# Kernel optimization log

Hardware: AMD Instinct MI355X
Metric: run time of the kernel (lower is better)

## Reference

```python
import jax, jax.numpy as jnp
import numpy as np

TEMPERATURE = 0.07
LAMBDA_CONTRASTIVE = 0.3
LAMBDA_CLASSIFICATION = 0.7
B = 8192
NUM_CLASSES = 57
EMBED_DIM = 256
NUM_TASKS = 57


def setup_inputs() -> dict:
    key = jax.random.key(0)
    k1, k2, k3, k4 = jax.random.split(key, 4)
    logits = jax.random.normal(k1, (B, NUM_CLASSES), dtype=jnp.float32)
    embeddings = jax.random.normal(k2, (B, EMBED_DIM), dtype=jnp.float32)
    labels = jax.random.randint(k3, (B,), 0, NUM_CLASSES, dtype=jnp.int64)
    task_ids = jax.random.randint(k4, (B,), 0, NUM_TASKS, dtype=jnp.int64)
    return {"logits": logits, "embeddings": embeddings, "labels": labels, "task_ids": task_ids}


def _forward(logits, embeddings, labels, task_ids):
    n, num_classes = logits.shape
    # --- classification loss (CrossEntropyLoss, mean) ---
    logp = jax.nn.log_softmax(logits, axis=-1)
    cls_loss = -jnp.take_along_axis(logp, labels[:, None], axis=1).squeeze(1).mean()
    # --- uncertainty: normalized entropy of softmax ---
    probs = jax.nn.softmax(logits, axis=-1)
    entropy = -jnp.sum(probs * jnp.log(probs + 1e-8), axis=-1)
    uncertainties = entropy / np.log(num_classes)
    # --- inter-task InfoNCE, uncertainty weighted ---
    norms = jnp.linalg.norm(embeddings, axis=-1, keepdims=True)
    e = embeddings / jnp.maximum(norms, 1e-12)  # F.normalize
    sim = jnp.matmul(e, e.T) / TEMPERATURE  # [B, B]
    eye = jnp.eye(n, dtype=bool)
    same_task = task_ids[None, :] == task_ids[:, None]
    pos_mask = same_task & ~eye          # task_mask with diagonal removed
    neg_mask = (~same_task) & ~eye       # negative_mask with diagonal removed
    exps = jnp.exp(sim)
    neg_sum = jnp.sum(jnp.where(neg_mask, exps, 0.0), axis=1)  # [B]
    valid = (pos_mask.sum(axis=1) > 0) & (neg_mask.sum(axis=1) > 0)  # [B]
    # per (anchor i, positive j): -log(exp(s_ij) / (exp(s_ij) + neg_sum_i + 1e-8)) * u_i
    pair_loss = -jnp.log(exps / (exps + neg_sum[:, None] + 1e-8)) * uncertainties[:, None]
    m = pos_mask & valid[:, None]
    count = jnp.maximum(m.sum(), 1)
    contrastive = jnp.sum(jnp.where(m, pair_loss, 0.0)) / count
    contrastive = jnp.where(m.sum() > 0, contrastive, 0.0)
    total = LAMBDA_CLASSIFICATION * cls_loss + LAMBDA_CONTRASTIVE * contrastive
    return total


def reference(logits, embeddings, labels, task_ids):
    return _forward(logits, embeddings, labels, task_ids)
```

## Files before the change

### kernel.cpp

```cpp
#include <hip/hip_runtime.h>
#include <hip/hip_fp8.h>
#include <math.h>

#define BSZ   8192
#define NCLS  57
#define DIM   256
#define NTASK 57
#define INV_T (1.0f/0.07f)
#define GBM   64
#define GBN   32
#define NTILE (GBM * GBN)
#define FINB  256

typedef float f32x4 __attribute__((ext_vector_type(4)));
typedef long  lgx2  __attribute__((ext_vector_type(2)));

__device__ __forceinline__ void gload_lds16(const void* g, void* l) {
    __builtin_amdgcn_global_load_lds(
        (const __attribute__((address_space(1))) unsigned int*)g,
        (__attribute__((address_space(3))) unsigned int*)l, 16, 0, 0);
}

__global__ __launch_bounds__(256) void k_prep(
        const float* __restrict__ logits, const float* __restrict__ emb,
        const int* __restrict__ labels, float* __restrict__ u,
        float* __restrict__ cls_part, unsigned char* __restrict__ e,
        int* __restrict__ hdr) {
    __shared__ float scls[4];
    int wave = threadIdx.x >> 6;
    int lane = threadIdx.x & 63;
    int row  = blockIdx.x * 4 + wave;

    float v = (lane < NCLS) ? logits[row * NCLS + lane] : -3.0e38f;
    float m = v;
    #pragma unroll
    for (int s = 1; s < 64; s <<= 1) m = fmaxf(m, __shfl_xor(m, s));
    float ex = (lane < NCLS) ? __expf(v - m) : 0.0f;
    float se = ex;
    #pragma unroll
    for (int s = 1; s < 64; s <<= 1) se += __shfl_xor(se, s);
    float lse = m + logf(se);
    float p = ex / se;
    float term = (lane < NCLS) ? p * logf(p + 1e-8f) : 0.0f;
    float ent = term;
    #pragma unroll
    for (int s = 1; s < 64; s <<= 1) ent += __shfl_xor(ent, s);
    ent = -ent;
    int lab = labels[row];
    float vl = __shfl(v, lab);
    float cls = lse - vl;

    const float4* src = reinterpret_cast<const float4*>(emb + (size_t)row * DIM);
    float4 x = src[lane];
    float ss = x.x*x.x + x.y*x.y + x.z*x.z + x.w*x.w;
    #pragma unroll
    for (int s = 1; s < 64; s <<= 1) ss += __shfl_xor(ss, s);
    float sc = 1.0f / fmaxf(sqrtf(ss), 1e-12f);
    __hip_fp8_e4m3 f0(x.x * sc), f1(x.y * sc), f2(x.z * sc), f3(x.w * sc);
    uchar4 o;
    o.x = *reinterpret_cast<unsigned char*>(&f0);
    o.y = *reinterpret_cast<unsigned char*>(&f1);
    o.z = *reinterpret_cast<unsigned char*>(&f2);
    o.w = *reinterpret_cast<unsigned char*>(&f3);
    int kp = (lane >> 4) * 64 + ((lane >> 1) & 3) * 16 + ((lane >> 3) & 1) * 8
           + (lane & 1) * 4;
    *reinterpret_cast<uchar4*>(e + (size_t)row * DIM + kp) = o;

    if (lane == 0) {
        u[row] = ent / 4.04305127f;
        scls[wave] = cls;
    }
    if (blockIdx.x == 0 && threadIdx.x < 64) hdr[threadIdx.x] = 0;
    __syncthreads();
    if (threadIdx.x == 0) cls_part[blockIdx.x] = scls[0] + scls[1] + scls[2] + scls[3];
}

template<bool HD>
__device__ __forceinline__ void epi_accum(
        const f32x4 (&acc)[4][4], const unsigned char* ts, const int* ctb,
        int m0, int cbase, int h, int g, int lr,
        float (&T)[4], float (&P)[4], float (&S)[4]) {
    #pragma unroll
    for (int m = 0; m < 4; ++m) {
        unsigned rt4 = *reinterpret_cast<const unsigned*>(&ts[h * 64 + m * 16 + g * 4]);
        #pragma unroll
        for (int r = 0; r < 4; ++r) {
            int rt = (rt4 >> (8 * r)) & 255;
            #pragma unroll
            for (int f = 0; f < 4; ++f) {
                float sv = acc[m][f][r] * INV_T;
                float ev = __expf(sv);
                bool keep = true;
                if (HD)
                    keep = (m0 + h * 64 + m * 16 + g * 4 + r) != (cbase + f * 16 + lr);
                bool eq = (rt == ctb[f]) && keep;
                T[f] += keep ? ev : 0.0f;
                P[f] += eq ? ev : 0.0f;
                S[f] += eq ? sv : 0.0f;
            }
        }
    }
}

__global__ __launch_bounds__(512, 2) void k_negsum(
        const unsigned char* __restrict__ E, const int* __restrict__ tasks,
        float* __restrict__ partial, int* __restrict__ task_count) {
    __shared__ unsigned char Asm[128 * 256];
    __shared__ unsigned char ts[128];
    __shared__ float scr[3][256];

    int b = (blockIdx.x & 7) * (NTILE / 8) + (blockIdx.x >> 3);
    int bm = b >> 5, bn = b & 31;
    int m0 = bm * 128, n0 = bn * 256;
    bool hasdiag = (bn == (bm >> 1));

    int tid = threadIdx.x;
    int w = tid >> 6, lane = tid & 63;
    int h = w >> 2, cg = w & 3;
    int g = lane >> 4, lr = lane & 15;
    int cbase = n0 + cg * 64;
    const unsigned char* bp = E + (size_t)(cbase + lr) * DIM + g * 16;

    lgx2 bc[4];
    #pragma unroll
    for (int f = 0; f < 4; ++f)
        bc[f] = *reinterpret_cast<const lgx2*>(bp + (size_t)f * 16 * DIM);

    #pragma unroll
    for (int it = 0; it < 4; ++it) {
        int flat = it * 512 + tid;
        int row = flat >> 4, kb = flat & 15;
        int kbs = kb ^ (row & 7);
        gload_lds16(E + (size_t)(m0 + row) * DIM + kbs * 16,
                    Asm + (size_t)(it * 512 + w * 64) * 16);
    }
    if (tid < 128) ts[tid] = (unsigned char)tasks[m0 + tid];
    __syncthreads();
    if (bn == 0 && tid < 128) atomicAdd(&task_count[ts[tid]], 1);

    f32x4 acc[4][4] = {};
    #pragma unroll 1
    for (int t = 0; t < 4; ++t) {
        lgx2 bn_[4];
        if (t < 3) {
            #pragma unroll
            for (int f = 0; f < 4; ++f)
                bn_[f] = *reinterpret_cast<const lgx2*>(
                    bp + (size_t)f * 16 * DIM + (t + 1) * 64);
        }
        lgx2 a[4];
        #pragma unroll
        for (int m = 0; m < 4; ++m)
            a[m] = *reinterpret_cast<const lgx2*>(
                Asm + (size_t)(h * 64 + m * 16 + lr) * 256
                    + (((t * 4 + g) ^ (lr & 7)) * 16));
        #pragma unroll
        for (int m = 0; m < 4; ++m)
            #pragma unroll
            for (int f = 0; f < 4; ++f) {
                acc[m][f] = __builtin_amdgcn_mfma_f32_16x16x32_fp8_fp8(
                    a[m][0], bc[f][0], acc[m][f], 0, 0, 0);
                acc[m][f] = __builtin_amdgcn_mfma_f32_16x16x32_fp8_fp8(
                    a[m][1], bc[f][1], acc[m][f], 0, 0, 0);
            }
        if (t < 3) {
            #pragma unroll
            for (int f = 0; f < 4; ++f) bc[f] = bn_[f];
        }
    }

    int ctb[4];
    #pragma unroll
    for (int f = 0; f < 4; ++f) ctb[f] = tasks[cbase + f * 16 + lr];
    float T[4] = {}, P[4] = {}, S[4] = {};
    if (hasdiag) epi_accum<true >(acc, ts, ctb, m0, cbase, h, g, lr, T, P, S);
    else         epi_accum<false>(acc, ts, ctb, m0, cbase, h, g, lr, T, P, S);

    #pragma unroll
    for (int f = 0; f < 4; ++f) {
        T[f] += __shfl_xor(T[f], 16); T[f] += __shfl_xor(T[f], 32);
        P[f] += __shfl_xor(P[f], 16); P[f] += __shfl_xor(P[f], 32);
        S[f] += __shfl_xor(S[f], 16); S[f] += __shfl_xor(S[f], 32);
    }
    if (h == 1 && g == 0) {
        #pragma unroll
        for (int f = 0; f < 4; ++f) {
            int c = cg * 64 + f * 16 + lr;
            scr[0][c] = T[f]; scr[1][c] = P[f]; scr[2][c] = S[f];
        }
    }
    __syncthreads();
    if (h == 0 && g == 0) {
        #pragma unroll
        for (int f = 0; f < 4; ++f) {
            int c = cg * 64 + f * 16 + lr;
            size_t sl = (size_t)bm * BSZ + n0 + c;
            partial[sl]                         = T[f] + scr[0][c];
            partial[(size_t)GBM * BSZ + sl]     = P[f] + scr[1][c];
            partial[(size_t)2 * GBM * BSZ + sl] = S[f] + scr[2][c];
        }
    }
}

__global__ __launch_bounds__(256) void k_finalize(
        const int* __restrict__ tasks, const int* __restrict__ task_count,
        const float* __restrict__ partial, const float* __restrict__ u,
        const float* __restrict__ cls_part, int* __restrict__ hdr,
        float* __restrict__ out) {
    __shared__ float sT[8][32], sP[8][32], sS[8][32];
    __shared__ float redf[4]; __shared__ long long redn[4];
    __shared__ int lastflag;

    int* ticket = hdr;
    float* contr_total = (float*)(hdr + 1);

    int tid = threadIdx.x;
    int c = tid & 31, q = tid >> 5;
    int j = blockIdx.x * 32 + c;

    float T = 0.0f, P = 0.0f, S = 0.0f;
    #pragma unroll
    for (int k = 0; k < 8; ++k) {
        int bm = q * 8 + k;
        size_t sl = (size_t)bm * BSZ + j;
        T += partial[sl];
        P += partial[(size_t)GBM * BSZ + sl];
        S += partial[(size_t)2 * GBM * BSZ + sl];
    }
    sT[q][c] = T; sP[q][c] = P; sS[q][c] = S;
    __syncthreads();

    if (tid < 32) {
        #pragma unroll
        for (int qq = 1; qq < 8; ++qq) {
            T = (qq == 1 ? sT[0][tid] : T) + sT[qq][tid];
            P = (qq == 1 ? sP[0][tid] : P) + sP[qq][tid];
            S = (qq == 1 ? sS[0][tid] : S) + sS[qq][tid];
        }
        int jj = blockIdx.x * 32 + tid;
        int cc = task_count[tasks[jj]];
        float v = 0.0f;
        if (cc >= 2 && cc < BSZ) {
            float C = (T - P) + 1e-8f;
            v = u[jj] * ((float)(cc - 1) * logf(C) + P / C - S);
        }
        #pragma unroll
        for (int s = 1; s < 32; s <<= 1) v += __shfl_xor(v, s);
        if (tid == 0) {
            atomicAdd(contr_total, v);
            __threadfence();
            lastflag = (__hip_atomic_fetch_add(ticket, 1, __ATOMIC_ACQ_REL,
                                               __HIP_MEMORY_SCOPE_AGENT) == FINB - 1);
        }
    }
    __syncthreads();
    if (!lastflag) return;
    __threadfence();

    float cl = 0.0f;
    for (int i = tid; i < BSZ / 4; i += 256) cl += cls_part[i];
    long long cn = 0;
    if (tid < NTASK) {
        int cc = task_count[tid];
        if (cc >= 2 && cc < BSZ) cn = (long long)cc * (cc - 1);
    }
    #pragma unroll
    for (int s = 1; s < 64; s <<= 1) { cl += __shfl_xor(cl, s); cn += __shfl_xor(cn, s); }
    int w = tid >> 6, lane = tid & 63;
    if (lane == 0) { redf[w] = cl; redn[w] = cn; }
    __syncthreads();
    if (tid == 0) {
        float ct = 0.0f; long long cnt = 0;
        #pragma unroll
        for (int qq = 0; qq < 4; ++qq) { ct += redf[qq]; cnt += redn[qq]; }
        float con = __hip_atomic_load(contr_total, __ATOMIC_ACQUIRE,
                                      __HIP_MEMORY_SCOPE_AGENT);
        out[0] = 0.7f * (ct / (float)BSZ)
               + 0.3f * (cnt > 0 ? con / (float)cnt : 0.0f);
    }
}

extern "C" void kernel_launch(void* const* d_in, const int* in_sizes, int n_in,
                              void* d_out, int out_size, void* d_ws, size_t ws_size,
                              hipStream_t stream) {
    const float* logits = (const float*)d_in[0];
    const float* emb    = (const float*)d_in[1];
    const int*   labels = (const int*)d_in[2];
    const int*   tasks  = (const int*)d_in[3];
    float* out = (float*)d_out;

    char* ws = (char*)d_ws;
    int*   hdr      = (int*)ws;
    int*   task_cnt = hdr + 2;
    float* u        = (float*)ws + 64;
    float* cls_part = u + BSZ;
    float* partial  = cls_part + 2048;
    unsigned char* e = (unsigned char*)(partial + (size_t)3 * GBM * BSZ);

    k_prep    <<<BSZ / 4, 256, 0, stream>>>(logits, emb, labels, u, cls_part, e, hdr);
    k_negsum  <<<NTILE,   512, 0, stream>>>(e, tasks, partial, task_cnt);
    k_finalize<<<FINB,    256, 0, stream>>>(tasks, task_cnt, partial, u, cls_part,
                                            hdr, out);
}
```

Baseline: 72.05 us.

## Halve row tile per block, raise occupancy, and use exp2 in epilogue

The negsum GEMM tile is cut from 128 to 64 rows per block, giving twice as many blocks. Smaller LDS and register footprints allow launch bounds of 8 blocks per SM instead of 2. The B-operand register prefetch is dropped in favour of loading directly inside the loop. The epilogue now uses exp2 with a pre-scaled constant and applies ln2 to S in finalize. In exchange, finalize reads twice as many partial rows, and more blocks reload the same B columns.

```diff
diff --git a/kernel.cpp b/kernel.cpp
--- a/kernel.cpp
+++ b/kernel.cpp
@@ -7,7 +7,9 @@
 #define DIM   256
 #define NTASK 57
 #define INV_T (1.0f/0.07f)
-#define GBM   64
+#define C2EXP (INV_T * 1.44269504f)
+#define LN2   0.69314718f
+#define GBM   128
 #define GBN   32
 #define NTILE (GBM * GBN)
 #define FINB  256
@@ -77,42 +79,42 @@
 
 template<bool HD>
 __device__ __forceinline__ void epi_accum(
-        const f32x4 (&acc)[4][4], const unsigned char* ts, const int* ctb,
+        const f32x4 (&acc)[2][4], const unsigned char* ts, const int* ctb,
         int m0, int cbase, int h, int g, int lr,
         float (&T)[4], float (&P)[4], float (&S)[4]) {
     #pragma unroll
-    for (int m = 0; m < 4; ++m) {
-        unsigned rt4 = *reinterpret_cast<const unsigned*>(&ts[h * 64 + m * 16 + g * 4]);
+    for (int m = 0; m < 2; ++m) {
+        unsigned rt4 = *reinterpret_cast<const unsigned*>(&ts[h * 32 + m * 16 + g * 4]);
         #pragma unroll
         for (int r = 0; r < 4; ++r) {
             int rt = (rt4 >> (8 * r)) & 255;
             #pragma unroll
             for (int f = 0; f < 4; ++f) {
-                float sv = acc[m][f][r] * INV_T;
-                float ev = __expf(sv);
+                float s2 = acc[m][f][r] * C2EXP;
+                float ev = exp2f(s2);
                 bool keep = true;
                 if (HD)
-                    keep = (m0 + h * 64 + m * 16 + g * 4 + r) != (cbase + f * 16 + lr);
+                    keep = (m0 + h * 32 + m * 16 + g * 4 + r) != (cbase + f * 16 + lr);
                 bool eq = (rt == ctb[f]) && keep;
                 T[f] += keep ? ev : 0.0f;
                 P[f] += eq ? ev : 0.0f;
-                S[f] += eq ? sv : 0.0f;
+                S[f] += eq ? s2 : 0.0f;
             }
         }
     }
 }
 
-__global__ __launch_bounds__(512, 2) void k_negsum(
+__global__ __launch_bounds__(512, 8) void k_negsum(
         const unsigned char* __restrict__ E, const int* __restrict__ tasks,
         float* __restrict__ partial, int* __restrict__ task_count) {
-    __shared__ unsigned char Asm[128 * 256];
-    __shared__ unsigned char ts[128];
+    __shared__ unsigned char Asm[64 * 256];
+    __shared__ unsigned char ts[64];
     __shared__ float scr[3][256];
 
     int b = (blockIdx.x & 7) * (NTILE / 8) + (blockIdx.x >> 3);
     int bm = b >> 5, bn = b & 31;
-    int m0 = bm * 128, n0 = bn * 256;
-    bool hasdiag = (bn == (bm >> 1));
+    int m0 = bm * 64, n0 = bn * 256;
+    bool hasdiag = (bn == (bm >> 2));
 
     int tid = threadIdx.x;
     int w = tid >> 6, lane = tid & 63;
@@ -121,51 +123,38 @@
     int cbase = n0 + cg * 64;
     const unsigned char* bp = E + (size_t)(cbase + lr) * DIM + g * 16;
 
-    lgx2 bc[4];
-    #pragma unroll
-    for (int f = 0; f < 4; ++f)
-        bc[f] = *reinterpret_cast<const lgx2*>(bp + (size_t)f * 16 * DIM);
-
-    #pragma unroll
-    for (int it = 0; it < 4; ++it) {
+    #pragma unroll
+    for (int it = 0; it < 2; ++it) {
         int flat = it * 512 + tid;
         int row = flat >> 4, kb = flat & 15;
         int kbs = kb ^ (row & 7);
         gload_lds16(E + (size_t)(m0 + row) * DIM + kbs * 16,
                     Asm + (size_t)(it * 512 + w * 64) * 16);
     }
-    if (tid < 128) ts[tid] = (unsigned char)tasks[m0 + tid];
-    __syncthreads();
-    if (bn == 0 && tid < 128) atomicAdd(&task_count[ts[tid]], 1);
-
-    f32x4 acc[4][4] = {};
+    if (tid < 64) ts[tid] = (unsigned char)tasks[m0 + tid];
+    __syncthreads();
+    if (bn == 0 && tid < 64) atomicAdd(&task_count[ts[tid]], 1);
+
+    f32x4 acc[2][4] = {};
     #pragma unroll 1
     for (int t = 0; t < 4; ++t) {
-        lgx2 bn_[4];
-        if (t < 3) {
+        lgx2 a[2];
+        #pragma unroll
+        for (int m = 0; m < 2; ++m)
+            a[m] = *reinterpret_cast<const lgx2*>(
+                Asm + (size_t)(h * 32 + m * 16 + lr) * 256
+                    + (((t * 4 + g) ^ (lr & 7)) * 16));
+        #pragma unroll
+        for (int f = 0; f < 4; ++f) {
+            lgx2 bc = *reinterpret_cast<const lgx2*>(
+                bp + (size_t)f * 16 * DIM + t * 64);
             #pragma unroll
-            for (int f = 0; f < 4; ++f)
-                bn_[f] = *reinterpret_cast<const lgx2*>(
-                    bp + (size_t)f * 16 * DIM + (t + 1) * 64);
-        }
-        lgx2 a[4];
-        #pragma unroll
-        for (int m = 0; m < 4; ++m)
-            a[m] = *reinterpret_cast<const lgx2*>(
-                Asm + (size_t)(h * 64 + m * 16 + lr) * 256
-                    + (((t * 4 + g) ^ (lr & 7)) * 16));
-        #pragma unroll
-        for (int m = 0; m < 4; ++m)
-            #pragma unroll
-            for (int f = 0; f < 4; ++f) {
+            for (int m = 0; m < 2; ++m) {
                 acc[m][f] = __builtin_amdgcn_mfma_f32_16x16x32_fp8_fp8(
-                    a[m][0], bc[f][0], acc[m][f], 0, 0, 0);
+                    a[m][0], bc[0], acc[m][f], 0, 0, 0);
                 acc[m][f] = __builtin_amdgcn_mfma_f32_16x16x32_fp8_fp8(
-                    a[m][1], bc[f][1], acc[m][f], 0, 0, 0);
+                    a[m][1], bc[1], acc[m][f], 0, 0, 0);
             }
-        if (t < 3) {
-            #pragma unroll
-            for (int f = 0; f < 4; ++f) bc[f] = bn_[f];
         }
     }
 
@@ -220,8 +209,8 @@
 
     float T = 0.0f, P = 0.0f, S = 0.0f;
     #pragma unroll
-    for (int k = 0; k < 8; ++k) {
-        int bm = q * 8 + k;
+    for (int k = 0; k < 16; ++k) {
+        int bm = q * 16 + k;
         size_t sl = (size_t)bm * BSZ + j;
         T += partial[sl];
         P += partial[(size_t)GBM * BSZ + sl];
@@ -242,7 +231,7 @@
         float v = 0.0f;
         if (cc >= 2 && cc < BSZ) {
             float C = (T - P) + 1e-8f;
-            v = u[jj] * ((float)(cc - 1) * logf(C) + P / C - S);
+            v = u[jj] * ((float)(cc - 1) * logf(C) + P / C - S * LN2);
         }
         #pragma unroll
         for (int s = 1; s < 32; s <<= 1) v += __shfl_xor(v, s);
```

After: 138.1 us. 91.7% more time.
